# Kernel optimization log

Hardware: AMD Instinct MI355X
Metric: run time of the kernel (lower is better)

## Reference

```python
import jax, jax.numpy as jnp
import numpy as np

B, H, W, C = 32, 32, 32, 768
E = 4          # num_experts
TOPK = 2
HD = int(C * 0.25)  # 192, expert hidden dim


def setup_inputs() -> dict:
    key = jax.random.key(0)
    ks = jax.random.split(key, 7)
    x = jax.random.normal(ks[0], (B, H, W, C), dtype=jnp.float32)
    # router: nn.Linear(C, E), weight [E, C] init N(0, 0.02), bias zeros
    router_w = jax.random.normal(ks[1], (E, C), dtype=jnp.float32) * 0.02
    router_b = jnp.zeros((E,), dtype=jnp.float32)
    # per-expert MLP: fc1 [E, HD, C], fc2 [E, C, HD] (torch Linear weight layout)
    fc1_w = jax.random.normal(ks[2], (E, HD, C), dtype=jnp.float32) * (1.0 / np.sqrt(C))
    fc1_b = jax.random.normal(ks[3], (E, HD), dtype=jnp.float32) * 0.01
    fc2_w = jax.random.normal(ks[4], (E, C, HD), dtype=jnp.float32) * (1.0 / np.sqrt(HD))
    fc2_b = jax.random.normal(ks[5], (E, C), dtype=jnp.float32) * 0.01
    return {"x": x, "router_w": router_w, "router_b": router_b,
            "fc1_w": fc1_w, "fc1_b": fc1_b, "fc2_w": fc2_w, "fc2_b": fc2_b}


def reference(x, router_w, router_b, fc1_w, fc1_b, fc2_w, fc2_b):
    b, h, w, c = x.shape
    xt = x.reshape(b, h * w, c)                              # [B, S, C]
    # --- router: softmax + top-k + renormalize ---
    logits = jnp.einsum('bsc,ec->bse', xt, router_w) + router_b
    probs = jax.nn.softmax(logits, axis=-1)                  # [B, S, E]
    topk_w, topk_idx = jax.lax.top_k(probs, TOPK)            # [B, S, K]
    topk_w = topk_w / (jnp.sum(topk_w, axis=-1, keepdims=True) + 1e-8)
    # per-expert combine weight: sum over k of weight where idx==e -> [B, S, E]
    combine = jnp.sum(jax.nn.one_hot(topk_idx, E, dtype=xt.dtype)
                      * topk_w[..., None], axis=-2)          # [B, S, E]
    # --- all experts densely (same math as masked gather/scatter) ---
    # fc1 + exact GELU: [B, S, E, HD]
    hmid = jax.nn.gelu(jnp.einsum('bsc,ehc->bseh', xt, fc1_w) + fc1_b,
                       approximate=False)
    # weight tokens before fc2 to avoid [B,S,E,C] intermediate
    hw = hmid * combine[..., None]                           # [B, S, E, HD]
    out = jnp.einsum('bseh,ech->bsc', hw, fc2_w)
    out = out + jnp.einsum('bse,ec->bsc', combine, fc2_b)    # weighted fc2 bias
    return out.reshape(b, h, w, c)
```

## Files before the change

### kernel.cpp

```cpp
#include <hip/hip_runtime.h>
#include <hip/hip_bf16.h>
#include <math.h>

typedef __attribute__((ext_vector_type(8))) __bf16 bf16x8;
typedef __attribute__((ext_vector_type(4))) float f32x4;
typedef __attribute__((ext_vector_type(4))) unsigned short u16x4;

#define TOKENS 32768
#define CDIM   768
#define SLOTCAP 33536
#define MT_TILES 262
#define RBLOCKS 1024

__device__ __forceinline__ void async_copy16(const void* g, void* l) {
    __builtin_amdgcn_global_load_lds(
        (const __attribute__((address_space(1))) void*)g,
        (__attribute__((address_space(3))) void*)l, 16, 0, 0);
}

__device__ __forceinline__ float fast_gelu(float v) {
    float x  = v * 0.70710678118654752f;
    float ax = fabsf(x);
    float t  = __builtin_amdgcn_rcpf(1.0f + 0.3275911f * ax);
    float poly = t * (0.254829592f +
                 t * (-0.284496736f +
                 t * (1.421413741f +
                 t * (-1.453152027f +
                 t * 1.061405429f))));
    float erfv = 1.0f - poly * __expf(-x * x);
    erfv = copysignf(erfv, x);
    return 0.5f * v * (1.0f + erfv);
}

__device__ __forceinline__ int pair_lo(int p) { return p < 3 ? 0 : (p < 5 ? 1 : 2); }
__device__ __forceinline__ int pair_hi(int p) { return p < 3 ? p + 1 : (p < 5 ? p - 1 : 3); }

__device__ __forceinline__ void bucket_offs(const int* __restrict__ meta, int* offs) {
    int run = 0;
#pragma unroll
    for (int p = 0; p < 6; ++p) {
        offs[p] = run;
        run += ((meta[p] + 127) >> 7) << 7;
    }
}

__global__ __launch_bounds__(256) void prep_weights(
    const float* __restrict__ fc1w, const float* __restrict__ fc2w,
    __hip_bfloat16* __restrict__ b1, __hip_bfloat16* __restrict__ b2t,
    int* __restrict__ slots, float2* __restrict__ swt, int* __restrict__ meta)
{
    int idx = blockIdx.x * 256 + threadIdx.x;
    if (idx < 32) meta[idx] = 0;
    if (idx < SLOTCAP) { slots[idx] = -1; swt[idx] = make_float2(0.f, 0.f); }
    b1[idx] = __float2bfloat16(fc1w[idx]);
    int c = idx / 768;
    int r = idx - c * 768;
    int e = r / 192;
    int h = r - e * 192;
    b2t[idx] = __float2bfloat16(fc2w[((size_t)e * 768 + c) * 192 + h]);
}

__global__ __launch_bounds__(256) void router_convert(
    const float* __restrict__ x, const float* __restrict__ rw,
    const float* __restrict__ rb,
    __hip_bfloat16* __restrict__ xb,
    int* __restrict__ pairid, float2* __restrict__ wpair, int* __restrict__ meta)
{
    __shared__ int rc[6];
    if (threadIdx.x < 6) rc[threadIdx.x] = 0;
    __syncthreads();

    const int wave = threadIdx.x >> 6;
    const int lane = threadIdx.x & 63;
    const int wid  = blockIdx.x * 4 + wave;
    const int el   = lane * 4;

    float4 wv[4][3];
#pragma unroll
    for (int e = 0; e < 4; ++e)
#pragma unroll
        for (int t = 0; t < 3; ++t)
            wv[e][t] = *(const float4*)(rw + e * CDIM + t * 256 + el);
    float rbv[4];
#pragma unroll
    for (int e = 0; e < 4; ++e) rbv[e] = rb[e];

    for (int it = 0; it < 8; ++it) {
        const int token = wid * 8 + it;
        const float* xr = x + (size_t)token * CDIM;

        float4 v[3];
#pragma unroll
        for (int t = 0; t < 3; ++t) v[t] = *(const float4*)(xr + t * 256 + el);

        unsigned short* xrow = (unsigned short*)xb + (size_t)token * CDIM;
#pragma unroll
        for (int t = 0; t < 3; ++t) {
            alignas(8) __hip_bfloat16 hb[4];
            hb[0] = __float2bfloat16(v[t].x);
            hb[1] = __float2bfloat16(v[t].y);
            hb[2] = __float2bfloat16(v[t].z);
            hb[3] = __float2bfloat16(v[t].w);
            *(u16x4*)(xrow + t * 256 + el) = *(const u16x4*)hb;
        }

        float s[4];
#pragma unroll
        for (int e = 0; e < 4; ++e) {
            s[e] = v[0].x * wv[e][0].x + v[0].y * wv[e][0].y
                 + v[0].z * wv[e][0].z + v[0].w * wv[e][0].w
                 + v[1].x * wv[e][1].x + v[1].y * wv[e][1].y
                 + v[1].z * wv[e][1].z + v[1].w * wv[e][1].w
                 + v[2].x * wv[e][2].x + v[2].y * wv[e][2].y
                 + v[2].z * wv[e][2].z + v[2].w * wv[e][2].w;
        }
#pragma unroll
        for (int e = 0; e < 4; ++e) {
            float vv = s[e];
            vv += __shfl_xor(vv, 32); vv += __shfl_xor(vv, 16); vv += __shfl_xor(vv, 8);
            vv += __shfl_xor(vv, 4);  vv += __shfl_xor(vv, 2);  vv += __shfl_xor(vv, 1);
            s[e] = vv;
        }
        float lg[4], p[4];
#pragma unroll
        for (int e = 0; e < 4; ++e) lg[e] = s[e] + rbv[e];
        float mx = fmaxf(fmaxf(lg[0], lg[1]), fmaxf(lg[2], lg[3]));
        float ps = 0.f;
#pragma unroll
        for (int e = 0; e < 4; ++e) { p[e] = __expf(lg[e] - mx); ps += p[e]; }
#pragma unroll
        for (int e = 0; e < 4; ++e) p[e] /= ps;
        int a = 0;
#pragma unroll
        for (int e = 1; e < 4; ++e) if (p[e] > p[a]) a = e;
        int b = (a == 0) ? 1 : 0;
#pragma unroll
        for (int e = 0; e < 4; ++e) if (e != a && p[e] > p[b]) b = e;
        float wsum = p[a] + p[b] + 1e-8f;
        if (lane == 0) {
            int lo = a < b ? a : b;
            int hi = a < b ? b : a;
            int pid = (lo == 0) ? hi - 1 : (lo == 1 ? hi + 1 : 5);
            pairid[token] = pid;
            wpair[token] = make_float2(p[lo] / wsum, p[hi] / wsum);
            atomicAdd(&rc[pid], 1);
        }
    }
    __syncthreads();
    if (threadIdx.x < 6 && rc[threadIdx.x])
        atomicAdd(&meta[threadIdx.x], rc[threadIdx.x]);
}

__global__ __launch_bounds__(256) void scatter_tokens(
    const int* __restrict__ pairid, const float2* __restrict__ wpair,
    int* __restrict__ slots, float2* __restrict__ swt, int* __restrict__ meta)
{
    __shared__ int sc[6], sb[6], soff[6];
    int tid = threadIdx.x;
    if (tid < 6) sc[tid] = 0;
    __syncthreads();
    int t = blockIdx.x * 256 + tid;
    int p = pairid[t];
    int r = atomicAdd(&sc[p], 1);
    __syncthreads();
    if (tid == 0) {
        int offs[6];
        bucket_offs(meta, offs);
#pragma unroll
        for (int q = 0; q < 6; ++q) soff[q] = offs[q];
    }
    if (tid < 6) sb[tid] = sc[tid] ? atomicAdd(&meta[16 + tid], sc[tid]) : 0;
    __syncthreads();
    int pos = soff[p] + sb[p] + r;
    slots[pos] = t;
    swt[pos] = wpair[t];
}

__global__ __launch_bounds__(256) void gather_rows(
    const __hip_bfloat16* __restrict__ xb, const int* __restrict__ slots,
    __hip_bfloat16* __restrict__ xg)
{
    int idx = blockIdx.x * 256 + threadIdx.x;
    int slot = idx / 96;
    int ch = idx - slot * 96;
    int tok = slots[slot];
    uint4 v = make_uint4(0u, 0u, 0u, 0u);
    if (tok >= 0)
        v = *(const uint4*)(xb + (size_t)tok * CDIM + ch * 8);
    *(uint4*)(xg + (size_t)slot * CDIM + ch * 8) = v;
}

#define BM 128
#define BN 128
#define BK 64

__global__ __launch_bounds__(256) void fc1_moe(
    const __hip_bfloat16* __restrict__ A,
    const __hip_bfloat16* __restrict__ Bt,
    const float2* __restrict__ swt,
    const int* __restrict__ meta, const float* __restrict__ bias1,
    __hip_bfloat16* __restrict__ HW)
{
    __shared__ __hip_bfloat16 smem[BM * BK * 4];

    const int tid = threadIdx.x;
    const int wave = tid >> 6, lane = tid & 63;
    const int wm = (wave >> 1) * 64, wn = (wave & 1) * 64;
    const int lrow = lane & 15, quad = lane >> 4;

    constexpr int NT = 3;
    constexpr int nwg = MT_TILES * NT;
    constexpr int q = nwg >> 3, rr = nwg & 7;
    const int bid = blockIdx.x;
    const int xcd = bid & 7, sidx = bid >> 3;
    const int wg = (xcd < rr ? xcd * (q + 1) : rr * (q + 1) + (xcd - rr) * q) + sidx;
    const int by = wg / NT;
    const int bx = wg - by * NT;
    const int rowB0 = bx * BN;
    const int rowA0 = by * BM;

    int offs[6];
    bucket_offs(meta, offs);
    int pb = 0;
#pragma unroll
    for (int i = 1; i < 6; ++i) pb += (rowA0 >= offs[i]) ? 1 : 0;
    const int lo = pair_lo(pb), hi = pair_hi(pb);

    const int srow = lane >> 3;
    const int scol = ((lane & 7) ^ srow) * 8;

    size_t aoff[4], boff[4];
    __hip_bfloat16* ldsA[4];
#pragma unroll
    for (int p = 0; p < 4; ++p) {
        int c = wave * 4 + p;
        int arow = c * 8 + srow;
        aoff[p] = (size_t)(rowA0 + arow) * 768 + scol;
        int grow = rowB0 + arow;
        int gb = (grow < 192) ? lo * 192 + grow : hi * 192 + (grow - 192);
        boff[p] = (size_t)gb * 768 + scol;
        ldsA[p] = smem + c * 8 * BK;
    }

    auto stage = [&](int buf, int k0) {
        int bo = buf * (2 * BM * BK);
#pragma unroll
        for (int p = 0; p < 4; ++p) {
            async_copy16(A + aoff[p] + k0, ldsA[p] + bo);
            async_copy16(Bt + boff[p] + k0, ldsA[p] + bo + BM * BK);
        }
    };

    f32x4 acc[4][4] = {};
    constexpr int NIT = 768 / BK;

    stage(0, 0);
    __syncthreads();
#pragma unroll
    for (int it = 0; it < NIT; ++it) {
        if (it + 1 < NIT) stage((it + 1) & 1, (it + 1) * BK);
        const __hip_bfloat16* As = smem + (it & 1) * (2 * BM * BK);
        const __hip_bfloat16* Bs = As + BM * BK;
#pragma unroll
        for (int kk = 0; kk < BK; kk += 32) {
            bf16x8 af[4], bfr[4];
#pragma unroll
            for (int i = 0; i < 4; ++i) {
                int row = wm + i * 16 + lrow;
                int gp = ((kk >> 3) + quad) ^ (lrow & 7);
                af[i] = *(const bf16x8*)(&As[row * BK + gp * 8]);
            }
#pragma unroll
            for (int j = 0; j < 4; ++j) {
                int row = wn + j * 16 + lrow;
                int gp = ((kk >> 3) + quad) ^ (lrow & 7);
                bfr[j] = *(const bf16x8*)(&Bs[row * BK + gp * 8]);
            }
#pragma unroll
            for (int i = 0; i < 4; ++i)
#pragma unroll
                for (int j = 0; j < 4; ++j)
                    acc[i][j] = __builtin_amdgcn_mfma_f32_16x16x32_bf16(
                        af[i], bfr[j], acc[i][j], 0, 0, 0);
        }
        __syncthreads();
    }

    const bool hf = (rowB0 + wn) >= 192;
    float b1v[4];
#pragma unroll
    for (int j = 0; j < 4; ++j) {
        int col = rowB0 + wn + j * 16 + lrow;
        int ng = (col < 192) ? lo * 192 + col : hi * 192 + (col - 192);
        b1v[j] = bias1[ng];
    }
#pragma unroll
    for (int i = 0; i < 4; ++i) {
#pragma unroll
        for (int r = 0; r < 4; ++r) {
            int rowl = wm + i * 16 + quad * 4 + r;
            float2 wv = swt[rowA0 + rowl];
            float cwt = hf ? wv.y : wv.x;
            __hip_bfloat16* srow_p = &smem[rowl * BN + wn + lrow];
#pragma unroll
            for (int j = 0; j < 4; ++j) {
                float v = fast_gelu(acc[i][j][r] + b1v[j]) * cwt;
                srow_p[j * 16] = __float2bfloat16(v);
            }
        }
    }
    __syncthreads();
#pragma unroll
    for (int t = 0; t < 8; ++t) {
        int idx = t * 256 + tid;
        int row = idx >> 4;
        int c16 = (idx & 15) * 8;
        *(uint4*)(HW + (size_t)(rowA0 + row) * 384 + rowB0 + c16) =
            *(const uint4*)(&smem[row * BN + c16]);
    }
}

__global__ __launch_bounds__(256) void fc2_moe(
    const __hip_bfloat16* __restrict__ A,
    const __hip_bfloat16* __restrict__ Bt,
    const int* __restrict__ slots, const float2* __restrict__ swt,
    const int* __restrict__ meta, const float* __restrict__ bias2,
    float* __restrict__ OUT)
{
    __shared__ __hip_bfloat16 smem[BM * BK * 4];

    const int tid = threadIdx.x;
    const int wave = tid >> 6, lane = tid & 63;
    const int wm = (wave >> 1) * 64, wn = (wave & 1) * 64;
    const int lrow = lane & 15, quad = lane >> 4;

    constexpr int NT = 6;
    constexpr int nwg = MT_TILES * NT;
    constexpr int q = nwg >> 3, rr = nwg & 7;
    const int bid = blockIdx.x;
    const int xcd = bid & 7, sidx = bid >> 3;
    const int wg = (xcd < rr ? xcd * (q + 1) : rr * (q + 1) + (xcd - rr) * q) + sidx;
    const int by = wg / NT;
    const int bx = wg - by * NT;
    const int rowB0 = bx * BN;
    const int rowA0 = by * BM;

    int offs[6];
    bucket_offs(meta, offs);
    int pb = 0;
#pragma unroll
    for (int i = 1; i < 6; ++i) pb += (rowA0 >= offs[i]) ? 1 : 0;
    const int lo = pair_lo(pb), hi = pair_hi(pb);

    const int srow = lane >> 3;
    const int scol = ((lane & 7) ^ srow) * 8;

    size_t aoff[4], boff[4];
    __hip_bfloat16* ldsA[4];
#pragma unroll
    for (int p = 0; p < 4; ++p) {
        int c = wave * 4 + p;
        int arow = c * 8 + srow;
        aoff[p] = (size_t)(rowA0 + arow) * 384 + scol;
        boff[p] = (size_t)(rowB0 + arow) * 768 + scol;
        ldsA[p] = smem + c * 8 * BK;
    }

    auto stage = [&](int buf, int k0) {
        int bo = buf * (2 * BM * BK);
        size_t badd = (size_t)(k0 < 192 ? lo * 192 : hi * 192 - 192) + k0;
#pragma unroll
        for (int p = 0; p < 4; ++p) {
            async_copy16(A + aoff[p] + k0, ldsA[p] + bo);
            async_copy16(Bt + boff[p] + badd, ldsA[p] + bo + BM * BK);
        }
    };

    f32x4 acc[4][4] = {};
    constexpr int NIT = 384 / BK;

    stage(0, 0);
    __syncthreads();
#pragma unroll
    for (int it = 0; it < NIT; ++it) {
        if (it + 1 < NIT) stage((it + 1) & 1, (it + 1) * BK);
        const __hip_bfloat16* As = smem + (it & 1) * (2 * BM * BK);
        const __hip_bfloat16* Bs = As + BM * BK;
#pragma unroll
        for (int kk = 0; kk < BK; kk += 32) {
            bf16x8 af[4], bfr[4];
#pragma unroll
            for (int i = 0; i < 4; ++i) {
                int row = wm + i * 16 + lrow;
                int gp = ((kk >> 3) + quad) ^ (lrow & 7);
                af[i] = *(const bf16x8*)(&As[row * BK + gp * 8]);
            }
#pragma unroll
            for (int j = 0; j < 4; ++j) {
                int row = wn + j * 16 + lrow;
                int gp = ((kk >> 3) + quad) ^ (lrow & 7);
                bfr[j] = *(const bf16x8*)(&Bs[row * BK + gp * 8]);
            }
#pragma unroll
            for (int i = 0; i < 4; ++i)
#pragma unroll
                for (int j = 0; j < 4; ++j)
                    acc[i][j] = __builtin_amdgcn_mfma_f32_16x16x32_bf16(
                        af[i], bfr[j], acc[i][j], 0, 0, 0);
        }
        __syncthreads();
    }

    float blo[4], bhi[4];
#pragma unroll
    for (int j = 0; j < 4; ++j) {
        int col = rowB0 + wn + j * 16 + lrow;
        blo[j] = bias2[lo * 768 + col];
        bhi[j] = bias2[hi * 768 + col];
    }
    float* smf = (float*)smem;
#pragma unroll
    for (int i = 0; i < 4; ++i) {
#pragma unroll
        for (int r = 0; r < 4; ++r) {
            int rowl = wm + i * 16 + quad * 4 + r;
            float2 wv = swt[rowA0 + rowl];
            float* sr = smf + rowl * BN + wn + lrow;
#pragma unroll
            for (int j = 0; j < 4; ++j)
                sr[j * 16] = acc[i][j][r] + wv.x * blo[j] + wv.y * bhi[j];
        }
    }
    __syncthreads();
#pragma unroll
    for (int t = 0; t < 16; ++t) {
        int idx = t * 256 + tid;
        int row = idx >> 5;
        int ch  = idx & 31;
        int tok = slots[rowA0 + row];
        if (tok >= 0)
            *(float4*)(OUT + (size_t)tok * CDIM + rowB0 + ch * 4) =
                *(const float4*)(smf + row * BN + ch * 4);
    }
}

extern "C" void kernel_launch(void* const* d_in, const int* in_sizes, int n_in,
                              void* d_out, int out_size, void* d_ws, size_t ws_size,
                              hipStream_t stream)
{
    const float* x    = (const float*)d_in[0];
    const float* rw   = (const float*)d_in[1];
    const float* rb   = (const float*)d_in[2];
    const float* fc1w = (const float*)d_in[3];
    const float* fc1b = (const float*)d_in[4];
    const float* fc2w = (const float*)d_in[5];
    const float* fc2b = (const float*)d_in[6];
    float* out = (float*)d_out;

    char* ws = (char*)d_ws;
    __hip_bfloat16* xb   = (__hip_bfloat16*)(ws);
    __hip_bfloat16* xg   = (__hip_bfloat16*)(ws + 50331648);
    __hip_bfloat16* hw   = (__hip_bfloat16*)(ws + 101842944);
    __hip_bfloat16* b1   = (__hip_bfloat16*)(ws + 127598592);
    __hip_bfloat16* b2t  = (__hip_bfloat16*)(ws + 128778240);
    float2*         wpr  = (float2*)       (ws + 129957888);
    float2*         swt  = (float2*)       (ws + 130220032);
    int*            pid  = (int*)          (ws + 130488320);
    int*            slots= (int*)          (ws + 130619392);
    int*            meta = (int*)          (ws + 130753536);

    prep_weights<<<2304, 256, 0, stream>>>(fc1w, fc2w, b1, b2t, slots, swt, meta);
    router_convert<<<RBLOCKS, 256, 0, stream>>>(x, rw, rb, xb, pid, wpr, meta);
    scatter_tokens<<<TOKENS / 256, 256, 0, stream>>>(pid, wpr, slots, swt, meta);
    gather_rows<<<SLOTCAP * 96 / 256, 256, 0, stream>>>(xb, slots, xg);

    fc1_moe<<<MT_TILES * 3, 256, 0, stream>>>(
        xg, b1, swt, meta, fc1b, hw);
    fc2_moe<<<MT_TILES * 6, 256, 0, stream>>>(
        hw, b2t, slots, swt, meta, fc2b, out);
}
```

Baseline: 294.1 us.

## Fuse token gather into fc1 loads and single-buffer LDS in MoE GEMMs

Removes the separate gather_rows kernel and the gathered activation buffer. fc1 now reads each A row straight from the bf16 token matrix through the slot index, with padded slots clamped to token 0. Both GEMMs drop double buffering and halve their LDS, which may allow more resident workgroups but gives up overlap of global loads with MFMA work. The fc2 epilogue is staged through LDS in two 64-row halves so it fits the smaller buffer.

Result: faster. 279.0 us (-5.1%).

```diff
diff --git a/kernel.cpp b/kernel.cpp
--- a/kernel.cpp
+++ b/kernel.cpp
@@ -176,20 +176,6 @@
     swt[pos] = wpair[t];
 }
 
-__global__ __launch_bounds__(256) void gather_rows(
-    const __hip_bfloat16* __restrict__ xb, const int* __restrict__ slots,
-    __hip_bfloat16* __restrict__ xg)
-{
-    int idx = blockIdx.x * 256 + threadIdx.x;
-    int slot = idx / 96;
-    int ch = idx - slot * 96;
-    int tok = slots[slot];
-    uint4 v = make_uint4(0u, 0u, 0u, 0u);
-    if (tok >= 0)
-        v = *(const uint4*)(xb + (size_t)tok * CDIM + ch * 8);
-    *(uint4*)(xg + (size_t)slot * CDIM + ch * 8) = v;
-}
-
 #define BM 128
 #define BN 128
 #define BK 64
@@ -197,11 +183,11 @@
 __global__ __launch_bounds__(256) void fc1_moe(
     const __hip_bfloat16* __restrict__ A,
     const __hip_bfloat16* __restrict__ Bt,
-    const float2* __restrict__ swt,
+    const int* __restrict__ slots, const float2* __restrict__ swt,
     const int* __restrict__ meta, const float* __restrict__ bias1,
     __hip_bfloat16* __restrict__ HW)
 {
-    __shared__ __hip_bfloat16 smem[BM * BK * 4];
+    __shared__ __hip_bfloat16 smem[BM * BK * 2];
 
     const int tid = threadIdx.x;
     const int wave = tid >> 6, lane = tid & 63;
@@ -235,32 +221,32 @@
     for (int p = 0; p < 4; ++p) {
         int c = wave * 4 + p;
         int arow = c * 8 + srow;
-        aoff[p] = (size_t)(rowA0 + arow) * 768 + scol;
+        int tok = slots[rowA0 + arow];
+        tok = tok < 0 ? 0 : tok;
+        aoff[p] = (size_t)tok * 768 + scol;
         int grow = rowB0 + arow;
         int gb = (grow < 192) ? lo * 192 + grow : hi * 192 + (grow - 192);
         boff[p] = (size_t)gb * 768 + scol;
         ldsA[p] = smem + c * 8 * BK;
     }
 
-    auto stage = [&](int buf, int k0) {
-        int bo = buf * (2 * BM * BK);
+    auto stage = [&](int k0) {
 #pragma unroll
         for (int p = 0; p < 4; ++p) {
-            async_copy16(A + aoff[p] + k0, ldsA[p] + bo);
-            async_copy16(Bt + boff[p] + k0, ldsA[p] + bo + BM * BK);
+            async_copy16(A + aoff[p] + k0, ldsA[p]);
+            async_copy16(Bt + boff[p] + k0, ldsA[p] + BM * BK);
         }
     };
 
     f32x4 acc[4][4] = {};
     constexpr int NIT = 768 / BK;
 
-    stage(0, 0);
-    __syncthreads();
 #pragma unroll
     for (int it = 0; it < NIT; ++it) {
-        if (it + 1 < NIT) stage((it + 1) & 1, (it + 1) * BK);
-        const __hip_bfloat16* As = smem + (it & 1) * (2 * BM * BK);
-        const __hip_bfloat16* Bs = As + BM * BK;
+        stage(it * BK);
+        __syncthreads();
+        const __hip_bfloat16* As = smem;
+        const __hip_bfloat16* Bs = smem + BM * BK;
 #pragma unroll
         for (int kk = 0; kk < BK; kk += 32) {
             bf16x8 af[4], bfr[4];
@@ -327,7 +313,7 @@
     const int* __restrict__ meta, const float* __restrict__ bias2,
     float* __restrict__ OUT)
 {
-    __shared__ __hip_bfloat16 smem[BM * BK * 4];
+    __shared__ __hip_bfloat16 smem[BM * BK * 2];
 
     const int tid = threadIdx.x;
     const int wave = tid >> 6, lane = tid & 63;
@@ -366,26 +352,24 @@
         ldsA[p] = smem + c * 8 * BK;
     }
 
-    auto stage = [&](int buf, int k0) {
-        int bo = buf * (2 * BM * BK);
+    auto stage = [&](int k0) {
         size_t badd = (size_t)(k0 < 192 ? lo * 192 : hi * 192 - 192) + k0;
 #pragma unroll
         for (int p = 0; p < 4; ++p) {
-            async_copy16(A + aoff[p] + k0, ldsA[p] + bo);
-            async_copy16(Bt + boff[p] + badd, ldsA[p] + bo + BM * BK);
+            async_copy16(A + aoff[p] + k0, ldsA[p]);
+            async_copy16(Bt + boff[p] + badd, ldsA[p] + BM * BK);
         }
     };
 
     f32x4 acc[4][4] = {};
     constexpr int NIT = 384 / BK;
 
-    stage(0, 0);
-    __syncthreads();
 #pragma unroll
     for (int it = 0; it < NIT; ++it) {
-        if (it + 1 < NIT) stage((it + 1) & 1, (it + 1) * BK);
-        const __hip_bfloat16* As = smem + (it & 1) * (2 * BM * BK);
-        const __hip_bfloat16* Bs = As + BM * BK;
+        stage(it * BK);
+        __syncthreads();
+        const __hip_bfloat16* As = smem;
+        const __hip_bfloat16* Bs = smem + BM * BK;
 #pragma unroll
         for (int kk = 0; kk < BK; kk += 32) {
             bf16x8 af[4], bfr[4];
@@ -420,27 +404,33 @@
     }
     float* smf = (float*)smem;
 #pragma unroll
-    for (int i = 0; i < 4; ++i) {
-#pragma unroll
-        for (int r = 0; r < 4; ++r) {
-            int rowl = wm + i * 16 + quad * 4 + r;
-            float2 wv = swt[rowA0 + rowl];
-            float* sr = smf + rowl * BN + wn + lrow;
-#pragma unroll
-            for (int j = 0; j < 4; ++j)
-                sr[j * 16] = acc[i][j][r] + wv.x * blo[j] + wv.y * bhi[j];
-        }
-    }
-    __syncthreads();
-#pragma unroll
-    for (int t = 0; t < 16; ++t) {
-        int idx = t * 256 + tid;
-        int row = idx >> 5;
-        int ch  = idx & 31;
-        int tok = slots[rowA0 + row];
-        if (tok >= 0)
-            *(float4*)(OUT + (size_t)tok * CDIM + rowB0 + ch * 4) =
-                *(const float4*)(smf + row * BN + ch * 4);
+    for (int h = 0; h < 2; ++h) {
+        if ((wave >> 1) == h) {
+#pragma unroll
+            for (int i = 0; i < 4; ++i) {
+#pragma unroll
+                for (int r = 0; r < 4; ++r) {
+                    int rowl = wm + i * 16 + quad * 4 + r;
+                    float2 wv = swt[rowA0 + rowl];
+                    float* sr = smf + (rowl - h * 64) * BN + wn + lrow;
+#pragma unroll
+                    for (int j = 0; j < 4; ++j)
+                        sr[j * 16] = acc[i][j][r] + wv.x * blo[j] + wv.y * bhi[j];
+                }
+            }
+        }
+        __syncthreads();
+#pragma unroll
+        for (int t = 0; t < 8; ++t) {
+            int idx = t * 256 + tid;
+            int row = idx >> 5;
+            int ch  = idx & 31;
+            int tok = slots[rowA0 + h * 64 + row];
+            if (tok >= 0)
+                *(float4*)(OUT + (size_t)tok * CDIM + rowB0 + ch * 4) =
+                    *(const float4*)(smf + row * BN + ch * 4);
+        }
+        __syncthreads();
     }
 }
 
@@ -459,23 +449,21 @@
 
     char* ws = (char*)d_ws;
     __hip_bfloat16* xb   = (__hip_bfloat16*)(ws);
-    __hip_bfloat16* xg   = (__hip_bfloat16*)(ws + 50331648);
-    __hip_bfloat16* hw   = (__hip_bfloat16*)(ws + 101842944);
-    __hip_bfloat16* b1   = (__hip_bfloat16*)(ws + 127598592);
-    __hip_bfloat16* b2t  = (__hip_bfloat16*)(ws + 128778240);
-    float2*         wpr  = (float2*)       (ws + 129957888);
-    float2*         swt  = (float2*)       (ws + 130220032);
-    int*            pid  = (int*)          (ws + 130488320);
-    int*            slots= (int*)          (ws + 130619392);
-    int*            meta = (int*)          (ws + 130753536);
+    __hip_bfloat16* hw   = (__hip_bfloat16*)(ws + 50331648);
+    __hip_bfloat16* b1   = (__hip_bfloat16*)(ws + 76087296);
+    __hip_bfloat16* b2t  = (__hip_bfloat16*)(ws + 77266944);
+    float2*         wpr  = (float2*)       (ws + 78446592);
+    float2*         swt  = (float2*)       (ws + 78708736);
+    int*            pid  = (int*)          (ws + 78977024);
+    int*            slots= (int*)          (ws + 79108096);
+    int*            meta = (int*)          (ws + 79242240);
 
     prep_weights<<<2304, 256, 0, stream>>>(fc1w, fc2w, b1, b2t, slots, swt, meta);
     router_convert<<<RBLOCKS, 256, 0, stream>>>(x, rw, rb, xb, pid, wpr, meta);
     scatter_tokens<<<TOKENS / 256, 256, 0, stream>>>(pid, wpr, slots, swt, meta);
-    gather_rows<<<SLOTCAP * 96 / 256, 256, 0, stream>>>(xb, slots, xg);
 
     fc1_moe<<<MT_TILES * 3, 256, 0, stream>>>(
-        xg, b1, swt, meta, fc1b, hw);
+        xb, b1, slots, swt, meta, fc1b, hw);
     fc2_moe<<<MT_TILES * 6, 256, 0, stream>>>(
         hw, b2t, slots, swt, meta, fc2b, out);
 }
```
